# Kernel optimization log

Measured on AMD Instinct MI355X. Metric: run time of the kernel, lower is better.

The kernel has to match this reference:

```python
import jax, jax.numpy as jnp
import numpy as np

BLOCK = 192
SCALE = 2048 ** (-0.5)


def setup_inputs() -> dict:
    key = jax.random.key(0)
    k1, k2, k3, k4 = jax.random.split(key, 4)
    B, N, C = 8, 1920, 512
    x = jax.random.normal(k1, (B, N, C), dtype=jnp.float32)
    g = jax.random.normal(k2, (B, N, C), dtype=jnp.float32)
    # nn.Linear(dim, dim, bias=False) weights, stored as [out, in] like torch
    Wq = jax.random.normal(k3, (C, C), dtype=jnp.float32) * (1.0 / np.sqrt(C))
    Wg = jax.random.normal(k4, (C, C), dtype=jnp.float32) * (1.0 / np.sqrt(C))
    return {"x": x, "g": g, "Wq": Wq, "Wg": Wg}


def reference(x, g, Wq, Wg):
    B, N, C = g.shape
    # q = x + mean over tokens of g
    q = x + jnp.mean(g, axis=1, keepdims=True)
    rel_q = jnp.einsum('bnc,dc->bnd', q, Wq)  # Linear: y = x @ W^T
    # ---- block-local cosine attention over chunks of 192 tokens ----
    gb = g.reshape(B * N // BLOCK, BLOCK, C)
    norm = jnp.linalg.norm(gb, axis=-1, keepdims=True)
    rel = gb / jnp.maximum(norm, 1e-12)  # F.normalize(dim=-1)
    scores = jnp.einsum('bic,bjc->bij', rel, rel) * SCALE  # [nb,192,192]
    attn = jax.nn.softmax(scores, axis=-1)
    g2 = jnp.einsum('bij,bjc->bic', attn, gb).reshape(B, N, C)
    # ---- global cross attention ----
    rel_g = jnp.einsum('bnc,dc->bnd', g2, Wg)
    scores2 = jnp.einsum('bmc,bnc->bmn', rel_q, rel_g) * SCALE  # [B,M,N]
    attn2 = jax.nn.softmax(scores2, axis=-1)
    out = jnp.einsum('bmn,bnc->bmc', attn2, g2)
    return out
```

## Files before the change

### kernel.cpp

```cpp
#include <hip/hip_runtime.h>
#include <math.h>

constexpr int Bsz  = 8;
constexpr int Ntok = 1920;
constexpr int Cdim = 512;
constexpr int BLK  = 192;
constexpr int Mrows = Bsz * Ntok;
constexpr int NBLK  = Mrows / BLK;
constexpr float SCALE = 0.02209708691207961f;

typedef _Float16 half8 __attribute__((ext_vector_type(8)));
typedef float    f32x4 __attribute__((ext_vector_type(4)));

#define GLOAD_LDS16(gp, lp) __builtin_amdgcn_global_load_lds( \
    (const __attribute__((address_space(1))) void*)(gp),      \
    (__attribute__((address_space(3))) void*)(lp), 16, 0, 0)

__device__ inline unsigned short f2h(float f) {
    _Float16 h = (_Float16)f;
    return __builtin_bit_cast(unsigned short, h);
}
__device__ inline float h2f(unsigned short u) {
    return (float)__builtin_bit_cast(_Float16, u);
}

template<int BK> __device__ inline int smask(int r) {
    return (BK == 32) ? ((r & 3) ^ ((r >> 2) & 3)) : (r & 7);
}

template<int N> __device__ __forceinline__ void vm_wait() {
    if constexpr (N == 0)      asm volatile("s_waitcnt vmcnt(0)" ::: "memory");
    else if constexpr (N == 2) asm volatile("s_waitcnt vmcnt(2)" ::: "memory");
    else if constexpr (N == 4) asm volatile("s_waitcnt vmcnt(4)" ::: "memory");
    else if constexpr (N == 6) asm volatile("s_waitcnt vmcnt(6)" ::: "memory");
    else                       asm volatile("s_waitcnt vmcnt(8)" ::: "memory");
}

__global__ void mean_partial(const float* __restrict__ g, float* __restrict__ part) {
    int b = blockIdx.x, t = blockIdx.y, c = threadIdx.x;
    const float* p = g + ((size_t)b * Ntok + (size_t)t * 48) * Cdim + c;
    float s = 0.f;
    #pragma unroll 4
    for (int n = 0; n < 48; ++n) s += p[(size_t)n * Cdim];
    part[((size_t)b * 40 + t) * Cdim + c] = s;
}

__global__ void mean_final(const float* __restrict__ part, float* __restrict__ meang) {
    int b = blockIdx.x, c = threadIdx.x;
    float s = 0.f;
    for (int t = 0; t < 40; ++t) s += part[((size_t)b * 40 + t) * Cdim + c];
    meang[b * Cdim + c] = s * (1.0f / (float)Ntok);
}

__global__ void invnorm_k(const float* __restrict__ g, float* __restrict__ invn) {
    int wid = threadIdx.x >> 6, lane = threadIdx.x & 63;
    int row = blockIdx.x * 4 + wid;
    const float* p = g + (size_t)row * Cdim;
    float ss = 0.f;
    #pragma unroll
    for (int i = lane; i < Cdim; i += 64) { float v = p[i]; ss += v * v; }
    #pragma unroll
    for (int o = 1; o < 64; o <<= 1) ss += __shfl_xor(ss, o);
    if (lane == 0) {
        float n = sqrtf(ss);
        invn[row] = 1.0f / fmaxf(n, 1e-12f);
    }
}

__global__ void cvt_k(const float* __restrict__ src, const float* __restrict__ bias,
                      unsigned short* __restrict__ dst, int n4) {
    int i = blockIdx.x * 256 + threadIdx.x;
    if (i >= n4) return;
    float4 v = ((const float4*)src)[i];
    if (bias) {
        int b  = i / (Ntok * Cdim / 4);
        int c4 = (i & (Cdim / 4 - 1)) << 2;
        float4 bv = *(const float4*)&bias[b * Cdim + c4];
        v.x += bv.x; v.y += bv.y; v.z += bv.z; v.w += bv.w;
    }
    ushort4 h;
    h.x = f2h(v.x); h.y = f2h(v.y); h.z = f2h(v.z); h.w = f2h(v.w);
    ((ushort4*)dst)[i] = h;
}

__global__ __launch_bounds__(256) void transpose1(
    const unsigned short* __restrict__ in, unsigned short* __restrict__ out,
    int R, int C, long inB, long outB)
{
    int z = blockIdx.z;
    in  += (size_t)z * inB;
    out += (size_t)z * outB;
    __shared__ unsigned short th[64][68];
    int r0 = blockIdx.y * 64, c0 = blockIdx.x * 64;
    int tr = threadIdx.x >> 4, tc = (threadIdx.x & 15) * 4;
    for (int rr = tr; rr < 64; rr += 16) {
        ushort4 h = *(const ushort4*)&in[(size_t)(r0 + rr) * C + c0 + tc];
        th[tc + 0][rr] = h.x; th[tc + 1][rr] = h.y; th[tc + 2][rr] = h.z; th[tc + 3][rr] = h.w;
    }
    __syncthreads();
    for (int cc = tr; cc < 64; cc += 16) {
        ushort4 h = *(const ushort4*)&th[cc][tc];
        *(ushort4*)&out[(size_t)(c0 + cc) * R + r0 + tc] = h;
    }
}

template<int FM, int FN, int BK>
__global__ __launch_bounds__(256) void mfma_gemm(
    const unsigned short* __restrict__ A, const unsigned short* __restrict__ B,
    float* __restrict__ Of32, unsigned short* __restrict__ Oh,
    int N, int K, int ld,
    long aB, long bB, long oB,
    float alpha, const float* __restrict__ rs, const float* __restrict__ cs, int sB)
{
    constexpr int BM = FM * 32, BN = FN * 32;
    constexpr int RPC = 512 / BK;
    constexpr int LPR = BK / 8;
    constexpr int NCH = (BM + BN) / RPC;
    constexpr int CPW = NCH / 4;
    int z = blockIdx.z;

    int gx = gridDim.x;
    int nwg = gx * gridDim.y;
    int orig = blockIdx.y * gx + blockIdx.x;
    int q = nwg >> 3, r = nwg & 7;
    int xcd = orig & 7, idx = orig >> 3;
    int wgid = (xcd < r ? xcd * (q + 1) : r * (q + 1) + (xcd - r) * q) + idx;
    int m0 = (wgid / gx) * BM, n0 = (wgid % gx) * BN;

    __shared__ __align__(16) unsigned short As[2][BM * BK];
    __shared__ __align__(16) unsigned short Bs[2][BN * BK];

    int tid  = threadIdx.x;
    int lane = tid & 63, wid = tid >> 6;
    int wm = (wid >> 1) * (FM * 16), wn = (wid & 1) * (FN * 16);

    int srow = lane / LPR;
    int sgc  = (lane % LPR) ^ smask<BK>(srow);

    const unsigned short* csrc[CPW];
    unsigned short* cdst0[CPW];
    unsigned short* cdst1[CPW];
    #pragma unroll
    for (int i = 0; i < CPW; ++i) {
        int c = wid * CPW + i;
        if (c < BM / RPC) {
            csrc[i]  = A + (size_t)z * aB + (size_t)(m0 + c * RPC + srow) * ld + sgc * 8;
            cdst0[i] = &As[0][c * 512];
            cdst1[i] = &As[1][c * 512];
        } else {
            int cb = c - BM / RPC;
            csrc[i]  = B + (size_t)z * bB + (size_t)(n0 + cb * RPC + srow) * ld + sgc * 8;
            cdst0[i] = &Bs[0][cb * 512];
            cdst1[i] = &Bs[1][cb * 512];
        }
    }

    f32x4 acc[FM][FN] = {};
    int fr = lane & 15, kq = lane >> 4;

    const int nt = K / BK;
    #pragma unroll
    for (int i = 0; i < CPW; ++i) GLOAD_LDS16(csrc[i], cdst0[i]);
    #pragma unroll
    for (int i = 0; i < CPW; ++i) GLOAD_LDS16(csrc[i] + BK, cdst1[i]);

    for (int t = 0; t < nt; ++t) {
        int cur = t & 1;
        if (t + 1 < nt) vm_wait<CPW>(); else vm_wait<0>();
        __builtin_amdgcn_sched_barrier(0);
        __builtin_amdgcn_s_barrier();
        __builtin_amdgcn_sched_barrier(0);

        const unsigned short* Ab = As[cur];
        const unsigned short* Bb = Bs[cur];
        #pragma unroll
        for (int ks = 0; ks < BK / 32; ++ks) {
            int slot = ks * 4 + kq;
            half8 a[FM], b[FN];
            #pragma unroll
            for (int f = 0; f < FM; ++f) {
                int rr = wm + f * 16 + fr;
                a[f] = *(const half8*)&Ab[rr * BK + ((slot ^ smask<BK>(rr)) << 3)];
            }
            #pragma unroll
            for (int f = 0; f < FN; ++f) {
                int rr = wn + f * 16 + fr;
                b[f] = *(const half8*)&Bb[rr * BK + ((slot ^ smask<BK>(rr)) << 3)];
            }
            #pragma unroll
            for (int i = 0; i < FM; ++i)
                #pragma unroll
                for (int j = 0; j < FN; ++j)
                    acc[i][j] = __builtin_amdgcn_mfma_f32_16x16x32_f16(a[i], b[j], acc[i][j], 0, 0, 0);
        }

        __builtin_amdgcn_sched_barrier(0);
        __builtin_amdgcn_s_barrier();
        if (t + 2 < nt) {
            const int k2 = (t + 2) * BK;
            #pragma unroll
            for (int i = 0; i < CPW; ++i)
                GLOAD_LDS16(csrc[i] + k2, cur ? cdst1[i] : cdst0[i]);
        }
    }

    float* O          = Of32 ? Of32 + (size_t)z * oB : nullptr;
    unsigned short* H = Oh   ? Oh   + (size_t)z * oB : nullptr;
    int fq = lane >> 4;
    #pragma unroll
    for (int i = 0; i < FM; ++i) {
        #pragma unroll
        for (int r4 = 0; r4 < 4; ++r4) {
            int gm = m0 + wm + i * 16 + fq * 4 + r4;
            float rf = alpha * (rs ? rs[(size_t)z * sB + gm] : 1.0f);
            #pragma unroll
            for (int j = 0; j < FN; ++j) {
                int gn = n0 + wn + j * 16 + fr;
                float v = acc[i][j][r4] * rf * (cs ? cs[(size_t)z * sB + gn] : 1.0f);
                size_t off = (size_t)gm * N + gn;
                if (O) O[off] = v;
                else   H[off] = f2h(v);
            }
        }
    }
}

__global__ __launch_bounds__(512, 2) void gemm256(
    const unsigned short* __restrict__ A, const unsigned short* __restrict__ B,
    unsigned short* __restrict__ Oh,
    int M, int N, int K, int ld,
    long aB, long bB, long oB, float alpha)
{
    int z = blockIdx.z;
    int gx = gridDim.x;
    int nwg = gx * gridDim.y;
    int orig = blockIdx.y * gx + blockIdx.x;
    int q = nwg >> 3, r = nwg & 7;
    int xcd = orig & 7, idx = orig >> 3;
    int wgid = (xcd < r ? xcd * (q + 1) : r * (q + 1) + (xcd - r) * q) + idx;
    int m0 = (wgid / gx) * 256, n0 = (wgid % gx) * 256;

    __shared__ __align__(16) unsigned short As[2][256 * 64];
    __shared__ __align__(16) unsigned short Bs[2][256 * 64];

    int tid = threadIdx.x, lane = tid & 63, wid = tid >> 6;
    int wr = wid >> 2, wc = wid & 3;
    const unsigned short* Az = A + (size_t)z * aB;
    const unsigned short* Bz = B + (size_t)z * bB;

    int srow8 = lane >> 3;
    int sslot = (lane & 7) ^ srow8;

    auto stageT = [&](int t) {
        int cur = t & 1;
        const int koff = t * 64;
        #pragma unroll
        for (int i = 0; i < 4; ++i) {
            int c = wid * 4 + i;
            int rrow = c * 8 + srow8;
            int gr = min(m0 + rrow, M - 1);
            GLOAD_LDS16(Az + (size_t)gr * ld + koff + sslot * 8, &As[cur][c * 512]);
        }
        #pragma unroll
        for (int i = 0; i < 4; ++i) {
            int c = wid * 4 + i;
            int rrow = c * 8 + srow8;
            int gc = min(n0 + rrow, N - 1);
            GLOAD_LDS16(Bz + (size_t)gc * ld + koff + sslot * 8, &Bs[cur][c * 512]);
        }
    };

    f32x4 acc[8][4] = {};
    int fr = lane & 15, kq = lane >> 4;

    const int nt = K / 64;
    stageT(0);
    stageT(1);

    for (int t = 0; t < nt; ++t) {
        int cur = t & 1;
        if (t + 1 < nt) vm_wait<8>(); else vm_wait<0>();
        __builtin_amdgcn_sched_barrier(0);
        __builtin_amdgcn_s_barrier();
        __builtin_amdgcn_sched_barrier(0);

        const unsigned short* Ab = As[cur];
        const unsigned short* Bb = Bs[cur];
        __builtin_amdgcn_s_setprio(1);
        #pragma unroll
        for (int mh = 0; mh < 2; ++mh) {
            #pragma unroll
            for (int nh = 0; nh < 2; ++nh) {
                half8 a[4][2], b[2][2];
                #pragma unroll
                for (int mf = 0; mf < 4; ++mf) {
                    int rr = wr * 128 + mh * 64 + mf * 16 + fr;
                    #pragma unroll
                    for (int ks = 0; ks < 2; ++ks) {
                        int slot = (ks * 4 + kq) ^ (rr & 7);
                        a[mf][ks] = *(const half8*)&Ab[rr * 64 + slot * 8];
                    }
                }
                #pragma unroll
                for (int nf = 0; nf < 2; ++nf) {
                    int rr = wc * 64 + nh * 32 + nf * 16 + fr;
                    #pragma unroll
                    for (int ks = 0; ks < 2; ++ks) {
                        int slot = (ks * 4 + kq) ^ (rr & 7);
                        b[nf][ks] = *(const half8*)&Bb[rr * 64 + slot * 8];
                    }
                }
                #pragma unroll
                for (int mf = 0; mf < 4; ++mf)
                    #pragma unroll
                    for (int nf = 0; nf < 2; ++nf)
                        #pragma unroll
                        for (int ks = 0; ks < 2; ++ks)
                            acc[mh * 4 + mf][nh * 2 + nf] =
                                __builtin_amdgcn_mfma_f32_16x16x32_f16(
                                    a[mf][ks], b[nf][ks], acc[mh * 4 + mf][nh * 2 + nf], 0, 0, 0);
            }
        }
        __builtin_amdgcn_s_setprio(0);

        __builtin_amdgcn_sched_barrier(0);
        __builtin_amdgcn_s_barrier();
        __builtin_amdgcn_sched_barrier(0);
        if (t + 2 < nt) stageT(t + 2);
    }

    unsigned short* H = Oh + (size_t)z * oB;
    int fq = lane >> 4;
    #pragma unroll
    for (int mi = 0; mi < 8; ++mi) {
        #pragma unroll
        for (int r4 = 0; r4 < 4; ++r4) {
            int gm = m0 + wr * 128 + mi * 16 + fq * 4 + r4;
            if (gm >= M) continue;
            #pragma unroll
            for (int ni = 0; ni < 4; ++ni) {
                int gn = n0 + wc * 64 + ni * 16 + fr;
                if (gn >= N) continue;
                H[(size_t)gm * N + gn] = f2h(acc[mi][ni][r4] * alpha);
            }
        }
    }
}

__global__ __launch_bounds__(256) void softmax_h(unsigned short* __restrict__ P, int cols) {
    __shared__ float buf[1920];
    __shared__ float red[4];
    size_t row = blockIdx.x;
    unsigned short* p = P + row * (size_t)cols;
    int tid = threadIdx.x;
    int nq = cols >> 2;

    float lmax = -1e30f;
    for (int q = tid; q < nq; q += 256) {
        ushort4 h = ((const ushort4*)p)[q];
        float v0 = h2f(h.x), v1 = h2f(h.y), v2 = h2f(h.z), v3 = h2f(h.w);
        buf[q * 4 + 0] = v0; buf[q * 4 + 1] = v1;
        buf[q * 4 + 2] = v2; buf[q * 4 + 3] = v3;
        lmax = fmaxf(lmax, fmaxf(fmaxf(v0, v1), fmaxf(v2, v3)));
    }
    #pragma unroll
    for (int o = 1; o < 64; o <<= 1) lmax = fmaxf(lmax, __shfl_xor(lmax, o));
    if ((tid & 63) == 0) red[tid >> 6] = lmax;
    __syncthreads();
    float bmax = fmaxf(fmaxf(red[0], red[1]), fmaxf(red[2], red[3]));

    float lsum = 0.f;
    for (int c = tid; c < cols; c += 256) {
        float e = expf(buf[c] - bmax);
        buf[c] = e;
        lsum += e;
    }
    #pragma unroll
    for (int o = 1; o < 64; o <<= 1) lsum += __shfl_xor(lsum, o);
    __syncthreads();
    if ((tid & 63) == 0) red[tid >> 6] = lsum;
    __syncthreads();
    float inv = 1.0f / (red[0] + red[1] + red[2] + red[3]);

    for (int q = tid; q < nq; q += 256) {
        ushort4 h;
        h.x = f2h(buf[q * 4 + 0] * inv);
        h.y = f2h(buf[q * 4 + 1] * inv);
        h.z = f2h(buf[q * 4 + 2] * inv);
        h.w = f2h(buf[q * 4 + 3] * inv);
        ((ushort4*)p)[q] = h;
    }
}

extern "C" void kernel_launch(void* const* d_in, const int* in_sizes, int n_in,
                              void* d_out, int out_size, void* d_ws, size_t ws_size,
                              hipStream_t stream) {
    (void)in_sizes; (void)n_in; (void)out_size; (void)ws_size;
    const float* x  = (const float*)d_in[0];
    const float* g  = (const float*)d_in[1];
    const float* Wq = (const float*)d_in[2];
    const float* Wg = (const float*)d_in[3];
    float* out = (float*)d_out;

    const size_t GE = (size_t)Mrows * Cdim;
    char* ws = (char*)d_ws;
    size_t off = 0;
    auto alloc = [&](size_t bytes) { char* p = ws + off; off += (bytes + 255) & ~(size_t)255; return p; };

    float* meang = (float*)alloc(Bsz * Cdim * 4);
    float* part  = (float*)alloc(Bsz * 40 * Cdim * 4);
    float* invn  = (float*)alloc(Mrows * 4);
    unsigned short* gh   = (unsigned short*)alloc(GE * 2);
    unsigned short* gTh  = (unsigned short*)alloc(GE * 2);
    unsigned short* qh   = (unsigned short*)alloc(GE * 2);
    unsigned short* wqh  = (unsigned short*)alloc((size_t)Cdim * Cdim * 2);
    unsigned short* wgh  = (unsigned short*)alloc((size_t)Cdim * Cdim * 2);
    unsigned short* rqh  = (unsigned short*)alloc(GE * 2);
    unsigned short* rgh  = (unsigned short*)alloc(GE * 2);
    unsigned short* g2h  = (unsigned short*)alloc(GE * 2);
    unsigned short* sbh  = (unsigned short*)alloc((size_t)NBLK * BLK * BLK * 2);
    unsigned short* s2h  = (unsigned short*)alloc((size_t)Bsz * Ntok * Ntok * 2);
    unsigned short* g2Th = qh;

    mean_partial<<<dim3(Bsz, 40), 512, 0, stream>>>(g, part);
    mean_final<<<Bsz, 512, 0, stream>>>(part, meang);
    invnorm_k<<<Mrows / 4, 256, 0, stream>>>(g, invn);

    cvt_k<<<(int)(GE / 4 + 255) / 256, 256, 0, stream>>>(g, nullptr, gh, (int)(GE / 4));
    cvt_k<<<(int)(GE / 4 + 255) / 256, 256, 0, stream>>>(x, meang, qh, (int)(GE / 4));
    cvt_k<<<(Cdim * Cdim / 4) / 256, 256, 0, stream>>>(Wq, nullptr, wqh, Cdim * Cdim / 4);
    cvt_k<<<(Cdim * Cdim / 4) / 256, 256, 0, stream>>>(Wg, nullptr, wgh, Cdim * Cdim / 4);

    transpose1<<<dim3(Cdim / 64, BLK / 64, NBLK), 256, 0, stream>>>(
        gh, gTh, BLK, Cdim, (long)BLK * Cdim, (long)Cdim * BLK);

    mfma_gemm<2, 4, 64><<<dim3(Cdim / 128, Mrows / 64), 256, 0, stream>>>(
        qh, wqh, nullptr, rqh, Cdim, Cdim, Cdim, 0, 0, 0, 1.0f, nullptr, nullptr, 0);

    mfma_gemm<2, 2, 32><<<dim3(3, 3, NBLK), 256, 0, stream>>>(
        gh, gh, nullptr, sbh, BLK, Cdim, Cdim,
        (long)BLK * Cdim, (long)BLK * Cdim, (long)BLK * BLK,
        SCALE, invn, invn, BLK);

    softmax_h<<<NBLK * BLK, 256, 0, stream>>>(sbh, BLK);

    mfma_gemm<2, 4, 64><<<dim3(Cdim / 128, BLK / 64, NBLK), 256, 0, stream>>>(
        sbh, gTh, nullptr, g2h, Cdim, BLK, BLK,
        (long)BLK * BLK, (long)Cdim * BLK, (long)BLK * Cdim,
        1.0f, nullptr, nullptr, 0);

    transpose1<<<dim3(Cdim / 64, Ntok / 64, Bsz), 256, 0, stream>>>(
        g2h, g2Th, Ntok, Cdim, (long)Ntok * Cdim, (long)Cdim * Ntok);

    mfma_gemm<2, 4, 64><<<dim3(Cdim / 128, Mrows / 64), 256, 0, stream>>>(
        g2h, wgh, nullptr, rgh, Cdim, Cdim, Cdim, 0, 0, 0, 1.0f, nullptr, nullptr, 0);

    gemm256<<<dim3(8, 8, Bsz), 512, 0, stream>>>(
        rqh, rgh, s2h, Ntok, Ntok, Cdim, Cdim,
        (long)Ntok * Cdim, (long)Ntok * Cdim, (long)Ntok * Ntok, SCALE);

    softmax_h<<<Bsz * Ntok, 256, 0, stream>>>(s2h, Ntok);

    mfma_gemm<2, 4, 64><<<dim3(Cdim / 128, Ntok / 64, Bsz), 256, 0, stream>>>(
        s2h, g2Th, out, nullptr, Cdim, Ntok, Ntok,
        (long)Ntok * Ntok, (long)Cdim * Ntok, (long)Ntok * Cdim,
        1.0f, nullptr, nullptr, 0);
}
```

Baseline: 262.7 us.

## Interleave half-tile prefetch with quarter MFMA phases in gemm256; enlarge final GEMM tile

Restructures the gemm256 main loop into four quarter phases. Each phase loads fragments from LDS, issues half-tile global-to-LDS prefetches for the next k-steps, and runs its MFMA block, so global loads spread across the iteration instead of arriving as one burst. The final attention-times-values GEMM also switches to a taller 128-row tile with half as many row blocks. The cost is many more barriers and waitcnts per iteration, and fewer workgroups on the last GEMM.

```diff
diff --git a/kernel.cpp b/kernel.cpp
--- a/kernel.cpp
+++ b/kernel.cpp
@@ -251,82 +251,104 @@
     int srow8 = lane >> 3;
     int sslot = (lane & 7) ^ srow8;
 
-    auto stageT = [&](int t) {
-        int cur = t & 1;
+    auto stageA = [&](int t, int h) {
+        int buf = t & 1;
         const int koff = t * 64;
         #pragma unroll
-        for (int i = 0; i < 4; ++i) {
-            int c = wid * 4 + i;
-            int rrow = c * 8 + srow8;
-            int gr = min(m0 + rrow, M - 1);
-            GLOAD_LDS16(Az + (size_t)gr * ld + koff + sslot * 8, &As[cur][c * 512]);
-        }
-        #pragma unroll
-        for (int i = 0; i < 4; ++i) {
-            int c = wid * 4 + i;
-            int rrow = c * 8 + srow8;
-            int gc = min(n0 + rrow, N - 1);
-            GLOAD_LDS16(Bz + (size_t)gc * ld + koff + sslot * 8, &Bs[cur][c * 512]);
+        for (int j2 = 0; j2 < 2; ++j2) {
+            int j = wid * 2 + j2;
+            int c = (j < 8) ? (h * 8 + j) : (16 + h * 8 + (j - 8));
+            int gr = min(m0 + c * 8 + srow8, M - 1);
+            GLOAD_LDS16(Az + (size_t)gr * ld + koff + sslot * 8, &As[buf][c * 512]);
+        }
+    };
+    auto stageB = [&](int t, int h) {
+        int buf = t & 1;
+        const int koff = t * 64;
+        #pragma unroll
+        for (int j2 = 0; j2 < 2; ++j2) {
+            int j = wid * 2 + j2;
+            int c = (j >> 2) * 8 + h * 4 + (j & 3);
+            int gc = min(n0 + c * 8 + srow8, N - 1);
+            GLOAD_LDS16(Bz + (size_t)gc * ld + koff + sslot * 8, &Bs[buf][c * 512]);
         }
     };
 
     f32x4 acc[8][4] = {};
     int fr = lane & 15, kq = lane >> 4;
 
+    half8 aF[4][2], bF[2][2];
+    auto qloads = [&](int T, int mh, int nh) {
+        const unsigned short* Ab = &As[T & 1][0];
+        const unsigned short* Bb = &Bs[T & 1][0];
+        #pragma unroll
+        for (int mf = 0; mf < 4; ++mf) {
+            int rr = wr * 128 + mh * 64 + mf * 16 + fr;
+            #pragma unroll
+            for (int ks = 0; ks < 2; ++ks)
+                aF[mf][ks] = *(const half8*)&Ab[rr * 64 + (((ks * 4 + kq) ^ (rr & 7)) << 3)];
+        }
+        #pragma unroll
+        for (int nf = 0; nf < 2; ++nf) {
+            int rr = wc * 64 + nh * 32 + nf * 16 + fr;
+            #pragma unroll
+            for (int ks = 0; ks < 2; ++ks)
+                bF[nf][ks] = *(const half8*)&Bb[rr * 64 + (((ks * 4 + kq) ^ (rr & 7)) << 3)];
+        }
+    };
+    auto qmfma = [&](int mh, int nh) {
+        __builtin_amdgcn_s_setprio(1);
+        #pragma unroll
+        for (int mf = 0; mf < 4; ++mf)
+            #pragma unroll
+            for (int nf = 0; nf < 2; ++nf)
+                #pragma unroll
+                for (int ks = 0; ks < 2; ++ks)
+                    acc[mh * 4 + mf][nh * 2 + nf] =
+                        __builtin_amdgcn_mfma_f32_16x16x32_f16(
+                            aF[mf][ks], bF[nf][ks], acc[mh * 4 + mf][nh * 2 + nf], 0, 0, 0);
+        __builtin_amdgcn_s_setprio(0);
+    };
+    auto barrier = [&]() {
+        __builtin_amdgcn_sched_barrier(0);
+        __builtin_amdgcn_s_barrier();
+        __builtin_amdgcn_sched_barrier(0);
+    };
+    auto lgkm0 = [&]() {
+        asm volatile("s_waitcnt lgkmcnt(0)" ::: "memory");
+        __builtin_amdgcn_sched_barrier(0);
+    };
+
     const int nt = K / 64;
-    stageT(0);
-    stageT(1);
-
-    for (int t = 0; t < nt; ++t) {
-        int cur = t & 1;
-        if (t + 1 < nt) vm_wait<8>(); else vm_wait<0>();
-        __builtin_amdgcn_sched_barrier(0);
-        __builtin_amdgcn_s_barrier();
-        __builtin_amdgcn_sched_barrier(0);
-
-        const unsigned short* Ab = As[cur];
-        const unsigned short* Bb = Bs[cur];
-        __builtin_amdgcn_s_setprio(1);
-        #pragma unroll
-        for (int mh = 0; mh < 2; ++mh) {
-            #pragma unroll
-            for (int nh = 0; nh < 2; ++nh) {
-                half8 a[4][2], b[2][2];
-                #pragma unroll
-                for (int mf = 0; mf < 4; ++mf) {
-                    int rr = wr * 128 + mh * 64 + mf * 16 + fr;
-                    #pragma unroll
-                    for (int ks = 0; ks < 2; ++ks) {
-                        int slot = (ks * 4 + kq) ^ (rr & 7);
-                        a[mf][ks] = *(const half8*)&Ab[rr * 64 + slot * 8];
-                    }
-                }
-                #pragma unroll
-                for (int nf = 0; nf < 2; ++nf) {
-                    int rr = wc * 64 + nh * 32 + nf * 16 + fr;
-                    #pragma unroll
-                    for (int ks = 0; ks < 2; ++ks) {
-                        int slot = (ks * 4 + kq) ^ (rr & 7);
-                        b[nf][ks] = *(const half8*)&Bb[rr * 64 + slot * 8];
-                    }
-                }
-                #pragma unroll
-                for (int mf = 0; mf < 4; ++mf)
-                    #pragma unroll
-                    for (int nf = 0; nf < 2; ++nf)
-                        #pragma unroll
-                        for (int ks = 0; ks < 2; ++ks)
-                            acc[mh * 4 + mf][nh * 2 + nf] =
-                                __builtin_amdgcn_mfma_f32_16x16x32_f16(
-                                    a[mf][ks], b[nf][ks], acc[mh * 4 + mf][nh * 2 + nf], 0, 0, 0);
-            }
-        }
-        __builtin_amdgcn_s_setprio(0);
-
-        __builtin_amdgcn_sched_barrier(0);
-        __builtin_amdgcn_s_barrier();
-        __builtin_amdgcn_sched_barrier(0);
-        if (t + 2 < nt) stageT(t + 2);
+    stageA(0, 0); stageB(0, 0); stageA(0, 1); stageB(0, 1);
+    stageA(1, 0); stageB(1, 0);
+    vm_wait<8>();
+    barrier();
+
+    for (int T = 0; T < nt; ++T) {
+        bool n1 = (T + 1) < nt, n2 = (T + 2) < nt;
+        qloads(T, 0, 0);
+        if (n1) stageA(T + 1, 1);
+        barrier(); lgkm0();
+        qmfma(0, 0);
+        if (n1) vm_wait<6>(); else vm_wait<0>();
+        barrier();
+        qloads(T, 0, 1);
+        if (n1) stageB(T + 1, 1);
+        barrier(); lgkm0();
+        qmfma(0, 1);
+        barrier();
+        qloads(T, 1, 0);
+        if (n2) stageA(T + 2, 0);
+        barrier(); lgkm0();
+        qmfma(1, 0);
+        barrier();
+        qloads(T, 1, 1);
+        if (n2) stageB(T + 2, 0);
+        barrier(); lgkm0();
+        qmfma(1, 1);
+        if (n1) { if (n2) vm_wait<8>(); else vm_wait<4>(); }
+        barrier();
     }
 
     unsigned short* H = Oh + (size_t)z * oB;
@@ -461,7 +483,7 @@
 
     softmax_h<<<Bsz * Ntok, 256, 0, stream>>>(s2h, Ntok);
 
-    mfma_gemm<2, 4, 64><<<dim3(Cdim / 128, Ntok / 64, Bsz), 256, 0, stream>>>(
+    mfma_gemm<4, 4, 64><<<dim3(Cdim / 128, Ntok / 128, Bsz), 256, 0, stream>>>(
         s2h, g2Th, out, nullptr, Cdim, Ntok, Ntok,
         (long)Ntok * Ntok, (long)Cdim * Ntok, (long)Ntok * Cdim,
         1.0f, nullptr, nullptr, 0);
```

Result: no change. 262.8 us (+0.0%).
